# Optimization experiments

Hardware: AMD Instinct MI355X
Metric: run time of the kernel (lower is better)

## Reference

```python
import jax, jax.numpy as jnp
import numpy as np

B, S, D_IN, D_OUT, H = 2, 2048, 1024, 1024, 16
DH = D_OUT // H

def setup_inputs() -> dict:
    key = jax.random.key(0)
    ks = jax.random.split(key, 6)
    sc = 0.02
    return {
        'x': jax.random.normal(ks[0], (B, S, D_IN), dtype=jnp.float32),
        'Wq': jax.random.normal(ks[1], (D_IN, D_OUT), dtype=jnp.float32) * sc,
        'Wk': jax.random.normal(ks[2], (D_IN, D_OUT), dtype=jnp.float32) * sc,
        'Wv': jax.random.normal(ks[3], (D_IN, D_OUT), dtype=jnp.float32) * sc,
        'Wo': jax.random.normal(ks[4], (D_OUT, D_OUT), dtype=jnp.float32) * sc,
        'bo': jax.random.normal(ks[5], (D_OUT,), dtype=jnp.float32) * sc,
    }

def reference(x, Wq, Wk, Wv, Wo, bo):
    b, s, _ = x.shape
    # projections, split heads: (b, h, s, dh)
    q = (x @ Wq).reshape(b, s, H, DH).transpose(0, 2, 1, 3)
    k = (x @ Wk).reshape(b, s, H, DH).transpose(0, 2, 1, 3)
    v = (x @ Wv).reshape(b, s, H, DH).transpose(0, 2, 1, 3)
    scores = jnp.einsum('bhqd,bhkd->bhqk', q, k)
    causal = jnp.triu(jnp.ones((s, s), dtype=bool), k=1)
    scores = jnp.where(causal, -jnp.inf, scores)
    attn = jax.nn.softmax(scores / jnp.sqrt(jnp.float32(DH)), axis=-1)
    ctx = jnp.einsum('bhqk,bhkd->bhqd', attn, v)
    ctx = ctx.transpose(0, 2, 1, 3).reshape(b, s, D_OUT)
    return ctx @ Wo + bo
```

## Files before the change

### kernel.cpp

```cpp
#include <hip/hip_runtime.h>
#include <hip/hip_bf16.h>
#include <cstdint>

typedef __attribute__((ext_vector_type(8))) __bf16 bf16x8;
typedef __attribute__((ext_vector_type(4))) float f32x4;
typedef __attribute__((ext_vector_type(8))) unsigned short u16x8;
typedef __attribute__((ext_vector_type(4))) unsigned short u16x4;
typedef __attribute__((ext_vector_type(4))) unsigned int u32x4;

#define NEG_INF (-__builtin_inff())

__device__ __forceinline__ unsigned short f2bf(float f) {
    unsigned int u = __builtin_bit_cast(unsigned int, f);
    u += 0x7FFFu + ((u >> 16) & 1u);
    return (unsigned short)(u >> 16);
}
__device__ __forceinline__ float bf2f(unsigned short u) {
    return __builtin_bit_cast(float, (unsigned int)u << 16);
}

__device__ __forceinline__ void gload16(const void* g, void* l) {
    __builtin_amdgcn_global_load_lds(
        (__attribute__((address_space(1))) void*)(uintptr_t)g,
        (__attribute__((address_space(3))) void*)(uint32_t)(uintptr_t)l, 16, 0, 0);
}

__global__ void prep_kernel(const float* __restrict__ x, const float* __restrict__ W0,
                            const float* __restrict__ W1, const float* __restrict__ W2,
                            const float* __restrict__ W3, unsigned short* __restrict__ xb,
                            unsigned short* __restrict__ Wcat, unsigned short* __restrict__ Wot) {
    __shared__ float t[64][68];
    const int tid = threadIdx.x;
    const int z = blockIdx.z;
    if (z == 4) {
        const int base = (blockIdx.y * 16 + blockIdx.x) * 256 + tid;
        #pragma unroll
        for (int v = 0; v < 8; ++v) {
            size_t u = (size_t)v * 65536 + base;
            const float4* p = (const float4*)x + u * 2;
            float4 a = p[0], c = p[1];
            u16x8 o;
            o[0] = f2bf(a.x); o[1] = f2bf(a.y); o[2] = f2bf(a.z); o[3] = f2bf(a.w);
            o[4] = f2bf(c.x); o[5] = f2bf(c.y); o[6] = f2bf(c.z); o[7] = f2bf(c.w);
            ((u16x8*)xb)[u] = o;
        }
        return;
    }
    const float* src = (z == 0) ? W0 : (z == 1) ? W1 : (z == 2) ? W2 : W3;
    unsigned short* dst = (z < 3) ? (Wcat + (size_t)z * 1024 * 1024) : Wot;
    const int n0 = blockIdx.x * 64, k0 = blockIdx.y * 64;
    #pragma unroll
    for (int i = 0; i < 4; ++i) {
        int idx = i * 256 + tid;
        int kr = idx >> 4, c4 = idx & 15;
        *(float4*)&t[kr][c4 * 4] = *(const float4*)&src[(size_t)(k0 + kr) * 1024 + n0 + c4 * 4];
    }
    __syncthreads();
    #pragma unroll
    for (int i = 0; i < 2; ++i) {
        int idx = i * 256 + tid;
        int nr = idx >> 3, c8 = idx & 7;
        u16x8 o;
        #pragma unroll
        for (int j = 0; j < 8; ++j) o[j] = f2bf(t[c8 * 8 + j][nr]);
        *(u16x8*)&dst[(size_t)(n0 + nr) * 1024 + k0 + c8 * 8] = o;
    }
}

__global__ __launch_bounds__(256, 2)
void gemm_qkv_kernel(const unsigned short* __restrict__ A, const unsigned short* __restrict__ Bt,
                     unsigned short* __restrict__ Qb, unsigned short* __restrict__ Kb,
                     unsigned short* __restrict__ Vtb) {
    __shared__ unsigned short As[128 * 64];
    __shared__ unsigned short Bs[128 * 64];
    const int tid = threadIdx.x;
    const int w = tid >> 6, l = tid & 63;
    const int lr = l & 15, lg = l >> 4;
    const int wr = w >> 1, wc = w & 1;
    const int id = blockIdx.y * 24 + blockIdx.x;
    const int swz = (id & 7) * 96 + (id >> 3);
    const int m0 = (swz / 24) * 128;
    const int n0 = (swz % 24) * 128;
    const int K = 1024;

    f32x4 acc[4][4] = {};

    for (int k0 = 0; k0 < 1024; k0 += 64) {
        #pragma unroll
        for (int p = 0; p < 4; ++p) {
            int seg = p * 4 + w;
            int row = seg * 8 + (l >> 3);
            int c16 = (l & 7) ^ (row & 7);
            gload16(A  + (size_t)(m0 + row) * K + k0 + c16 * 8, &As[seg * 512]);
            gload16(Bt + (size_t)(n0 + row) * K + k0 + c16 * 8, &Bs[seg * 512]);
        }
        __syncthreads();
        #pragma unroll
        for (int ks = 0; ks < 2; ++ks) {
            bf16x8 af[4], bfr[4];
            #pragma unroll
            for (int i = 0; i < 4; ++i) {
                int ra = wr * 64 + i * 16 + lr;
                af[i] = *(const bf16x8*)&As[ra * 64 + (((ks << 2) | lg) ^ (ra & 7)) * 8];
                int rb = wc * 64 + i * 16 + lr;
                bfr[i] = *(const bf16x8*)&Bs[rb * 64 + (((ks << 2) | lg) ^ (rb & 7)) * 8];
            }
            #pragma unroll
            for (int i = 0; i < 4; ++i)
                #pragma unroll
                for (int j = 0; j < 4; ++j)
                    acc[i][j] = __builtin_amdgcn_mfma_f32_16x16x32_bf16(af[i], bfr[j], acc[i][j], 0, 0, 0);
        }
        __syncthreads();
    }

    const int seg = n0 >> 10;
    const int n0l = n0 & 1023;
    if (seg < 2) {
        unsigned short* C = (seg == 0) ? Qb : Kb;
        const float sc = (seg == 0) ? 0.125f * 1.44269504f : 1.0f;
        #pragma unroll
        for (int i = 0; i < 4; ++i)
            #pragma unroll
            for (int j = 0; j < 4; ++j) {
                int n = n0l + wc * 64 + j * 16 + lr;
                #pragma unroll
                for (int r = 0; r < 4; ++r) {
                    int m = m0 + wr * 64 + i * 16 + lg * 4 + r;
                    C[(size_t)m * 1024 + n] = f2bf(acc[i][j][r] * sc);
                }
            }
    } else {
        #pragma unroll
        for (int i = 0; i < 4; ++i)
            #pragma unroll
            for (int j = 0; j < 4; ++j) {
                int n = n0l + wc * 64 + j * 16 + lr;
                int mb = m0 + wr * 64 + i * 16 + lg * 4;
                int bb = mb >> 11, s = mb & 2047;
                int s6 = s & 63;
                int kp = (((s6 >> 4) & 1) << 5) | (((s6 >> 2) & 3) << 3) | (((s6 >> 5) & 1) << 2);
                int sp = (s & ~63) | kp;
                u16x4 o;
                #pragma unroll
                for (int r = 0; r < 4; ++r) o[r] = f2bf(acc[i][j][r]);
                *(u16x4*)&Vtb[((size_t)(bb * 1024 + n)) * 2048 + sp] = o;
            }
    }
}

static __device__ const unsigned char QS_TAB[24] = {
    7,15,14,14,13,6,12,5,
    15,13,12,10,11,10,11,9,
    0,1,2,3,8,8,9,4};
static __device__ const unsigned char TY_TAB[24] = {
    0,2,1,2,2,0,2,0,
    1,1,1,1,1,2,2,2,
    0,0,0,0,1,2,1,0};

__global__ __launch_bounds__(256, 4)
void flash_attn_kernel(const unsigned short* __restrict__ Q, const unsigned short* __restrict__ Kg,
                       const unsigned short* __restrict__ Vt, unsigned short* __restrict__ ctx,
                       unsigned short* __restrict__ P_O, float* __restrict__ P_l) {
    __shared__ unsigned short Ks[2][4096];
    __shared__ unsigned short Vs[2][4096];
    const int tid = threadIdx.x, w = tid >> 6, l = tid & 63;
    const int lr = l & 15, lg = l >> 4;

    const int level = blockIdx.x >> 5;
    const int bh = blockIdx.x & 31;
    const int qs = QS_TAB[level], ty = TY_TAB[level];
    const int Tf = 2 * qs + 2, mid = qs + 1;
    const int t0 = (ty == 2) ? mid : 0;
    const int t1 = (ty == 1) ? mid : Tf;
    const int b = bh >> 4, h = bh & 15;
    const int qw = qs * 128 + w * 32;

    const int srow8 = w * 8 + (l >> 3);
    const int scol  = (l & 7) ^ (srow8 & 7);
    const unsigned short* Kbase = Kg + (size_t)(b * 2048) * 1024 + h * 64;
    const unsigned short* Vbase = Vt + (size_t)(b * 1024 + h * 64) * 2048;

    const __bf16 one = (__bf16)1.0f;
    const bf16x8 ones = {one, one, one, one, one, one, one, one};

    bf16x8 qf[2][2];
    #pragma unroll
    for (int mi = 0; mi < 2; ++mi)
        #pragma unroll
        for (int ks = 0; ks < 2; ++ks)
            qf[mi][ks] = *(const bf16x8*)&Q[(size_t)(b * 2048 + qw + mi * 16 + lr) * 1024 + h * 64 + ks * 32 + lg * 8];

    f32x4 lacc[2] = {};
    f32x4 oacc[2][4] = {};

    #pragma unroll
    for (int p = 0; p < 2; ++p)
        gload16(Kbase + (size_t)(t0 * 64 + p * 32 + srow8) * 1024 + scol * 8, &Ks[0][(p * 32 + w * 8) * 64]);

    for (int t = t0; t < t1; ++t) {
        const int cur = (t - t0) & 1;
        const int k0 = t * 64;
        #pragma unroll
        for (int p = 0; p < 2; ++p)
            gload16(Vbase + (size_t)(p * 32 + srow8) * 2048 + k0 + scol * 8, &Vs[cur][(p * 32 + w * 8) * 64]);
        const int ktn = (t + 1 < t1) ? t + 1 : t0;
        #pragma unroll
        for (int p = 0; p < 2; ++p)
            gload16(Kbase + (size_t)(ktn * 64 + p * 32 + srow8) * 1024 + scol * 8, &Ks[cur ^ 1][(p * 32 + w * 8) * 64]);

        asm volatile("s_waitcnt vmcnt(4)" ::: "memory");
        __builtin_amdgcn_s_barrier();

        f32x4 sf[2][4] = {};
        __builtin_amdgcn_s_setprio(1);
        #pragma unroll
        for (int ks = 0; ks < 2; ++ks) {
            bf16x8 kf[4];
            #pragma unroll
            for (int ni = 0; ni < 4; ++ni) {
                int rk = ni * 16 + lr;
                kf[ni] = *(const bf16x8*)&Ks[cur][rk * 64 + (((ks << 2) | lg) ^ (rk & 7)) * 8];
            }
            #pragma unroll
            for (int ni = 0; ni < 4; ++ni)
                #pragma unroll
                for (int mi = 0; mi < 2; ++mi)
                    sf[mi][ni] = __builtin_amdgcn_mfma_f32_16x16x32_bf16(kf[ni], qf[mi][ks], sf[mi][ni], 0, 0, 0);
        }
        __builtin_amdgcn_s_setprio(0);

        u32x4 pa0u[2], pa1u[2];
        #pragma unroll
        for (int mi = 0; mi < 2; ++mi) {
            if (t >= Tf - 2) {
                #pragma unroll
                for (int ni = 0; ni < 4; ++ni)
                    #pragma unroll
                    for (int r = 0; r < 4; ++r)
                        if (k0 + ni * 16 + lg * 4 + r > qw + mi * 16 + lr) sf[mi][ni][r] = NEG_INF;
            }
            #pragma unroll
            for (int ni = 0; ni < 4; ++ni)
                #pragma unroll
                for (int r = 0; r < 4; ++r)
                    sf[mi][ni][r] = __builtin_amdgcn_exp2f(sf[mi][ni][r]);

            asm("v_cvt_pk_bf16_f32 %0, %1, %2" : "=v"(pa0u[mi][0]) : "v"(sf[mi][0][0]), "v"(sf[mi][0][1]));
            asm("v_cvt_pk_bf16_f32 %0, %1, %2" : "=v"(pa0u[mi][1]) : "v"(sf[mi][0][2]), "v"(sf[mi][0][3]));
            asm("v_cvt_pk_bf16_f32 %0, %1, %2" : "=v"(pa0u[mi][2]) : "v"(sf[mi][2][0]), "v"(sf[mi][2][1]));
            asm("v_cvt_pk_bf16_f32 %0, %1, %2" : "=v"(pa0u[mi][3]) : "v"(sf[mi][2][2]), "v"(sf[mi][2][3]));
            asm("v_cvt_pk_bf16_f32 %0, %1, %2" : "=v"(pa1u[mi][0]) : "v"(sf[mi][1][0]), "v"(sf[mi][1][1]));
            asm("v_cvt_pk_bf16_f32 %0, %1, %2" : "=v"(pa1u[mi][1]) : "v"(sf[mi][1][2]), "v"(sf[mi][1][3]));
            asm("v_cvt_pk_bf16_f32 %0, %1, %2" : "=v"(pa1u[mi][2]) : "v"(sf[mi][3][0]), "v"(sf[mi][3][1]));
            asm("v_cvt_pk_bf16_f32 %0, %1, %2" : "=v"(pa1u[mi][3]) : "v"(sf[mi][3][2]), "v"(sf[mi][3][3]));

            lacc[mi] = __builtin_amdgcn_mfma_f32_16x16x32_bf16(
                __builtin_bit_cast(bf16x8, pa0u[mi]), ones, lacc[mi], 0, 0, 0);
            lacc[mi] = __builtin_amdgcn_mfma_f32_16x16x32_bf16(
                __builtin_bit_cast(bf16x8, pa1u[mi]), ones, lacc[mi], 0, 0, 0);
        }

        asm volatile("s_waitcnt vmcnt(2)" ::: "memory");
        __builtin_amdgcn_s_barrier();

        __builtin_amdgcn_s_setprio(1);
        #pragma unroll
        for (int ks = 0; ks < 2; ++ks) {
            bf16x8 vb[4];
            #pragma unroll
            for (int ni = 0; ni < 4; ++ni) {
                int rv = ni * 16 + lr;
                vb[ni] = *(const bf16x8*)&Vs[cur][rv * 64 + (((ks << 2) | lg) ^ (rv & 7)) * 8];
            }
            #pragma unroll
            for (int mi = 0; mi < 2; ++mi) {
                bf16x8 pa = __builtin_bit_cast(bf16x8, ks ? pa1u[mi] : pa0u[mi]);
                #pragma unroll
                for (int ni = 0; ni < 4; ++ni)
                    oacc[mi][ni] = __builtin_amdgcn_mfma_f32_16x16x32_bf16(pa, vb[ni], oacc[mi][ni], 0, 0, 0);
            }
        }
        __builtin_amdgcn_s_setprio(0);
    }

    if (ty == 0) {
        #pragma unroll
        for (int mi = 0; mi < 2; ++mi)
            #pragma unroll
            for (int r = 0; r < 4; ++r) {
                float inv = 1.0f / lacc[mi][r];
                int q = qw + mi * 16 + lg * 4 + r;
                size_t base = (size_t)(b * 2048 + q) * 1024 + h * 64 + lr;
                #pragma unroll
                for (int ni = 0; ni < 4; ++ni)
                    ctx[base + ni * 16] = f2bf(oacc[mi][ni][r] * inv);
            }
    } else {
        const int pidx = ((qs - 8) * 32 + bh) * 2 + (ty - 1);
        unsigned short* po = P_O + (size_t)pidx * 8192;
        #pragma unroll
        for (int mi = 0; mi < 2; ++mi)
            #pragma unroll
            for (int r = 0; r < 4; ++r) {
                int rowl = w * 32 + mi * 16 + lg * 4 + r;
                #pragma unroll
                for (int ni = 0; ni < 4; ++ni)
                    po[rowl * 64 + ni * 16 + lr] = f2bf(oacc[mi][ni][r]);
            }
        if (lr == 0) {
            #pragma unroll
            for (int mi = 0; mi < 2; ++mi)
                #pragma unroll
                for (int r = 0; r < 4; ++r)
                    P_l[pidx * 128 + w * 32 + mi * 16 + lg * 4 + r] = lacc[mi][r];
        }
    }
}

__global__ __launch_bounds__(256)
void combine_kernel(const unsigned short* __restrict__ P_O, const float* __restrict__ P_l,
                    unsigned short* __restrict__ ctx) {
    const int qs = 8 + (blockIdx.x >> 5);
    const int bh = blockIdx.x & 31;
    const int b = bh >> 4, h = bh & 15;
    const int p0 = ((qs - 8) * 32 + bh) * 2, p1 = p0 + 1;
    const int t = threadIdx.x;
    const int row = t >> 1, half = t & 1;
    const float inv = 1.0f / (P_l[p0 * 128 + row] + P_l[p1 * 128 + row]);
    const u16x8* o0 = (const u16x8*)&P_O[(size_t)p0 * 8192 + row * 64 + half * 32];
    const u16x8* o1 = (const u16x8*)&P_O[(size_t)p1 * 8192 + row * 64 + half * 32];
    unsigned short* dst = ctx + (size_t)(b * 2048 + qs * 128 + row) * 1024 + h * 64 + half * 32;
    #pragma unroll
    for (int v = 0; v < 4; ++v) {
        u16x8 a = o0[v], c = o1[v], o;
        #pragma unroll
        for (int j = 0; j < 8; ++j)
            o[j] = f2bf((bf2f(a[j]) + bf2f(c[j])) * inv);
        ((u16x8*)dst)[v] = o;
    }
}

__global__ __launch_bounds__(256, 4)
void gemm_out_kernel(const unsigned short* __restrict__ A, const unsigned short* __restrict__ Bt,
                     float* __restrict__ C, const float* __restrict__ bias) {
    __shared__ unsigned short As[128 * 64];
    __shared__ unsigned short Bs[64 * 64];
    const int tid = threadIdx.x;
    const int w = tid >> 6, l = tid & 63;
    const int lr = l & 15, lg = l >> 4;
    const int wr = w >> 1, wc = w & 1;
    const int id = blockIdx.y * 16 + blockIdx.x;
    const int swz = (id & 7) * 64 + (id >> 3);
    const int m0 = (swz >> 4) * 128;
    const int n0 = (swz & 15) * 64;
    const int K = 1024;

    f32x4 acc[4][2] = {};

    for (int k0 = 0; k0 < 1024; k0 += 64) {
        #pragma unroll
        for (int p = 0; p < 4; ++p) {
            int seg = p * 4 + w;
            int row = seg * 8 + (l >> 3);
            int c16 = (l & 7) ^ (row & 7);
            gload16(A + (size_t)(m0 + row) * K + k0 + c16 * 8, &As[seg * 512]);
        }
        #pragma unroll
        for (int p = 0; p < 2; ++p) {
            int seg = p * 4 + w;
            int row = seg * 8 + (l >> 3);
            int c16 = (l & 7) ^ (row & 7);
            gload16(Bt + (size_t)(n0 + row) * K + k0 + c16 * 8, &Bs[seg * 512]);
        }
        __syncthreads();
        #pragma unroll
        for (int ks = 0; ks < 2; ++ks) {
            bf16x8 af[4], bfr[2];
            #pragma unroll
            for (int i = 0; i < 4; ++i) {
                int ra = wr * 64 + i * 16 + lr;
                af[i] = *(const bf16x8*)&As[ra * 64 + (((ks << 2) | lg) ^ (ra & 7)) * 8];
            }
            #pragma unroll
            for (int j = 0; j < 2; ++j) {
                int rb = wc * 32 + j * 16 + lr;
                bfr[j] = *(const bf16x8*)&Bs[rb * 64 + (((ks << 2) | lg) ^ (rb & 7)) * 8];
            }
            #pragma unroll
            for (int i = 0; i < 4; ++i)
                #pragma unroll
                for (int j = 0; j < 2; ++j)
                    acc[i][j] = __builtin_amdgcn_mfma_f32_16x16x32_bf16(af[i], bfr[j], acc[i][j], 0, 0, 0);
        }
        __syncthreads();
    }

    #pragma unroll
    for (int i = 0; i < 4; ++i)
        #pragma unroll
        for (int j = 0; j < 2; ++j) {
            int n = n0 + wc * 32 + j * 16 + lr;
            float bv = bias[n];
            #pragma unroll
            for (int r = 0; r < 4; ++r) {
                int m = m0 + wr * 64 + i * 16 + lg * 4 + r;
                C[(size_t)m * 1024 + n] = acc[i][j][r] + bv;
            }
        }
}

extern "C" void kernel_launch(void* const* d_in, const int* in_sizes, int n_in,
                              void* d_out, int out_size, void* d_ws, size_t ws_size,
                              hipStream_t stream) {
    (void)in_sizes; (void)n_in; (void)out_size; (void)ws_size;
    const float* x  = (const float*)d_in[0];
    const float* Wq = (const float*)d_in[1];
    const float* Wk = (const float*)d_in[2];
    const float* Wv = (const float*)d_in[3];
    const float* Wo = (const float*)d_in[4];
    const float* bo = (const float*)d_in[5];
    float* out = (float*)d_out;

    char* ws = (char*)d_ws;
    const size_t MB = 1024 * 1024;
    unsigned short* xb   = (unsigned short*)(ws);
    unsigned short* Wcat = (unsigned short*)(ws + 8  * MB);
    unsigned short* Wot  = (unsigned short*)(ws + 14 * MB);
    unsigned short* Qb   = (unsigned short*)(ws + 16 * MB);
    unsigned short* Kb   = (unsigned short*)(ws + 24 * MB);
    unsigned short* Vtb  = (unsigned short*)(ws + 32 * MB);
    unsigned short* Cxb  = (unsigned short*)(ws + 40 * MB);

    unsigned short* P_O  = (unsigned short*)(ws);
    float*          P_l  = (float*)(ws + 8 * MB);

    prep_kernel<<<dim3(16, 16, 5), 256, 0, stream>>>(x, Wq, Wk, Wv, Wo, xb, Wcat, Wot);
    gemm_qkv_kernel<<<dim3(24, 32), 256, 0, stream>>>(xb, Wcat, Qb, Kb, Vtb);
    flash_attn_kernel<<<768, 256, 0, stream>>>(Qb, Kb, Vtb, Cxb, P_O, P_l);
    combine_kernel<<<256, 256, 0, stream>>>(P_O, P_l, Cxb);
    gemm_out_kernel<<<dim3(16, 32), 256, 0, stream>>>(Cxb, Wot, out, bo);
}
```

Measured before the change: 84.79 us.

## Triple-buffer K/V tiles with two-ahead prefetch and one barrier per iteration

The flash-attention loop moves from double-buffered K with just-in-time V loads to a three-stage LDS ring. Both K and V tiles are prefetched two iterations ahead. This drops the second wait-and-barrier in each iteration and gives global loads more time to land before they are used. In exchange, LDS per block grows to 48KB and the launch bound drops from 4 to 3 blocks per CU, so occupancy falls.

```diff
diff --git a/kernel.cpp b/kernel.cpp
--- a/kernel.cpp
+++ b/kernel.cpp
@@ -158,12 +158,12 @@
     1,1,1,1,1,2,2,2,
     0,0,0,0,1,2,1,0};
 
-__global__ __launch_bounds__(256, 4)
+__global__ __launch_bounds__(256, 3)
 void flash_attn_kernel(const unsigned short* __restrict__ Q, const unsigned short* __restrict__ Kg,
                        const unsigned short* __restrict__ Vt, unsigned short* __restrict__ ctx,
                        unsigned short* __restrict__ P_O, float* __restrict__ P_l) {
-    __shared__ unsigned short Ks[2][4096];
-    __shared__ unsigned short Vs[2][4096];
+    __shared__ unsigned short Ks[3][4096];
+    __shared__ unsigned short Vs[3][4096];
     const int tid = threadIdx.x, w = tid >> 6, l = tid & 63;
     const int lr = l & 15, lg = l >> 4;
 
@@ -173,6 +173,7 @@
     const int Tf = 2 * qs + 2, mid = qs + 1;
     const int t0 = (ty == 2) ? mid : 0;
     const int t1 = (ty == 1) ? mid : Tf;
+    const int T = t1 - t0;
     const int b = bh >> 4, h = bh & 15;
     const int qw = qs * 128 + w * 32;
 
@@ -195,22 +196,32 @@
     f32x4 oacc[2][4] = {};
 
     #pragma unroll
-    for (int p = 0; p < 2; ++p)
-        gload16(Kbase + (size_t)(t0 * 64 + p * 32 + srow8) * 1024 + scol * 8, &Ks[0][(p * 32 + w * 8) * 64]);
-
-    for (int t = t0; t < t1; ++t) {
-        const int cur = (t - t0) & 1;
+    for (int u = 0; u < 2; ++u) {
+        int ts = (u < T) ? t0 + u : t0;
+        #pragma unroll
+        for (int p = 0; p < 2; ++p) {
+            gload16(Kbase + (size_t)(ts * 64 + p * 32 + srow8) * 1024 + scol * 8, &Ks[u][(p * 32 + w * 8) * 64]);
+            gload16(Vbase + (size_t)(p * 32 + srow8) * 2048 + ts * 64 + scol * 8, &Vs[u][(p * 32 + w * 8) * 64]);
+        }
+    }
+
+    for (int u = 0; u < T; ++u) {
+        const int t = t0 + u;
+        const int cur = u % 3;
         const int k0 = t * 64;
-        #pragma unroll
-        for (int p = 0; p < 2; ++p)
-            gload16(Vbase + (size_t)(p * 32 + srow8) * 2048 + k0 + scol * 8, &Vs[cur][(p * 32 + w * 8) * 64]);
-        const int ktn = (t + 1 < t1) ? t + 1 : t0;
-        #pragma unroll
-        for (int p = 0; p < 2; ++p)
-            gload16(Kbase + (size_t)(ktn * 64 + p * 32 + srow8) * 1024 + scol * 8, &Ks[cur ^ 1][(p * 32 + w * 8) * 64]);
 
         asm volatile("s_waitcnt vmcnt(4)" ::: "memory");
         __builtin_amdgcn_s_barrier();
+
+        {
+            const int nxt = (u + 2) % 3;
+            const int ts = (u + 2 < T) ? t + 2 : t0;
+            #pragma unroll
+            for (int p = 0; p < 2; ++p) {
+                gload16(Kbase + (size_t)(ts * 64 + p * 32 + srow8) * 1024 + scol * 8, &Ks[nxt][(p * 32 + w * 8) * 64]);
+                gload16(Vbase + (size_t)(p * 32 + srow8) * 2048 + ts * 64 + scol * 8, &Vs[nxt][(p * 32 + w * 8) * 64]);
+            }
+        }
 
         f32x4 sf[2][4] = {};
         __builtin_amdgcn_s_setprio(1);
@@ -260,9 +271,6 @@
             lacc[mi] = __builtin_amdgcn_mfma_f32_16x16x32_bf16(
                 __builtin_bit_cast(bf16x8, pa1u[mi]), ones, lacc[mi], 0, 0, 0);
         }
-
-        asm volatile("s_waitcnt vmcnt(2)" ::: "memory");
-        __builtin_amdgcn_s_barrier();
 
         __builtin_amdgcn_s_setprio(1);
         #pragma unroll
```

Measured after the change: 85.73 us. No clear change (+1.1%).
